# Kernel optimization log

Measured on AMD Instinct MI355X. Metric: run time of the kernel, lower is better.

## Reference

```python
import jax, jax.numpy as jnp
import numpy as np

N = 50000
E = 600000
LLM_DIM = 640
HIDDEN = 128
STRUCT_DIM = 16
N_STRUCT_TYPES = 5
N_LAYERS = 2
LN_EPS = 1e-5


def setup_inputs() -> dict:
    key = jax.random.key(0)
    ks = jax.random.split(key, 10)
    llm_feat = jax.random.normal(ks[0], (N, LLM_DIM), dtype=jnp.float32)
    struct_type_ids = jax.random.randint(ks[1], (N,), 0, N_STRUCT_TYPES, dtype=jnp.int64)
    edge_index = jax.random.randint(ks[2], (2, E), 0, N, dtype=jnp.int64)
    proj_out = HIDDEN - STRUCT_DIM  # 112
    proj_W = jax.random.normal(ks[3], (LLM_DIM, proj_out), dtype=jnp.float32) / np.sqrt(LLM_DIM)
    proj_b = jnp.zeros((proj_out,), dtype=jnp.float32)
    struct_emb = jax.random.normal(ks[4], (N_STRUCT_TYPES, STRUCT_DIM), dtype=jnp.float32)
    gcn_W = jax.random.normal(ks[5], (N_LAYERS, HIDDEN, HIDDEN), dtype=jnp.float32) / np.sqrt(HIDDEN)
    gcn_b = jnp.zeros((N_LAYERS, HIDDEN), dtype=jnp.float32)
    ln_g = jnp.ones((HIDDEN,), dtype=jnp.float32)
    ln_b = jnp.zeros((HIDDEN,), dtype=jnp.float32)
    return dict(llm_feat=llm_feat, struct_type_ids=struct_type_ids, edge_index=edge_index,
                proj_W=proj_W, proj_b=proj_b, struct_emb=struct_emb,
                gcn_W=gcn_W, gcn_b=gcn_b, ln_g=ln_g, ln_b=ln_b)


def _gcn_conv(x, src, dst, deg_inv_sqrt, W, b):
    """PyG GCNConv: x' = D^{-1/2}(A+I)D^{-1/2} (x W) + b, D over A+I."""
    xw = x @ W  # [N, H]
    norm = deg_inv_sqrt[src] * deg_inv_sqrt[dst]  # [E]
    msg = xw[src] * norm[:, None]  # [E, H]
    agg = jax.ops.segment_sum(msg, dst, num_segments=N)  # [N, H]
    # self-loop contribution: norm_ii = deg_i^{-1}
    agg = agg + xw * (deg_inv_sqrt * deg_inv_sqrt)[:, None]
    return agg + b


def reference(llm_feat, struct_type_ids, edge_index, proj_W, proj_b,
              struct_emb, gcn_W, gcn_b, ln_g, ln_b):
    x_llm = llm_feat @ proj_W + proj_b  # [N, hidden-struct_dim]
    x_struct = struct_emb[struct_type_ids]  # [N, struct_dim]
    x = jnp.concatenate([x_llm, x_struct], axis=-1)  # [N, hidden]

    src, dst = edge_index[0], edge_index[1]
    # degree with self-loops (A + I)
    deg = 1.0 + jax.ops.segment_sum(jnp.ones((E,), dtype=x.dtype), dst, num_segments=N)
    deg_inv_sqrt = jax.lax.rsqrt(deg)

    for l in range(N_LAYERS):
        x_new = jax.nn.relu(_gcn_conv(x, src, dst, deg_inv_sqrt, gcn_W[l], gcn_b[l]))
        # dropout is identity in eval mode
        x = x + x_new

    mean = jnp.mean(x, axis=-1, keepdims=True)
    var = jnp.mean(jnp.square(x - mean), axis=-1, keepdims=True)
    return (x - mean) * jax.lax.rsqrt(var + LN_EPS) * ln_g + ln_b
```

## Files before the change

kernel.cpp:

```cpp
#include <hip/hip_runtime.h>

#define N_NODES 50000
#define E_EDGES 600000
#define LLM_DIM 640
#define HIDDEN 128
#define POUT 112
#define NB_SCAN 98

typedef __attribute__((ext_vector_type(8))) short bf16x8;
typedef __attribute__((ext_vector_type(4))) float f32x4;

__device__ inline unsigned short f2bf(float f) {
    unsigned u = __float_as_uint(f);
    u += 0x7fff + ((u >> 16) & 1);
    return (unsigned short)(u >> 16);
}
__device__ inline float bflo(unsigned v) { return __uint_as_float(v << 16); }
__device__ inline float bfhi(unsigned v) { return __uint_as_float(v & 0xffff0000u); }

__global__ void deg_count(const int* __restrict__ eidx, int* __restrict__ cnt) {
    int e = blockIdx.x * 256 + threadIdx.x;
    if (e < E_EDGES) atomicAdd(&cnt[eidx[E_EDGES + e]], 1);
}

__global__ void make_dis(const int* __restrict__ cnt, float* __restrict__ dis) {
    int i = blockIdx.x * 256 + threadIdx.x;
    if (i < N_NODES) dis[i] = rsqrtf(1.0f + (float)cnt[i]);
}

__global__ __launch_bounds__(256) void scan_blocksum(const int* __restrict__ cnt, int* __restrict__ bsum) {
    __shared__ int s[256];
    int b = blockIdx.x, t = threadIdx.x;
    int i0 = b * 512 + t, i1 = i0 + 256;
    int v = (i0 < N_NODES ? cnt[i0] : 0) + (i1 < N_NODES ? cnt[i1] : 0);
    s[t] = v;
    __syncthreads();
    for (int st = 128; st; st >>= 1) {
        if (t < st) s[t] += s[t + st];
        __syncthreads();
    }
    if (t == 0) bsum[b] = s[0];
}

__global__ void scan_bsum(const int* __restrict__ bsum, int* __restrict__ bpre) {
    __shared__ int s[128];
    int t = threadIdx.x;
    if (t < NB_SCAN) s[t] = bsum[t];
    __syncthreads();
    if (t == 0) {
        int a = 0;
        for (int i = 0; i < NB_SCAN; i++) { int v = s[i]; s[i] = a; a += v; }
    }
    __syncthreads();
    if (t < NB_SCAN) bpre[t] = s[t];
}

__global__ __launch_bounds__(256) void scan_offs(const int* __restrict__ cnt, const int* __restrict__ bpre,
                                                 int* __restrict__ offs) {
    __shared__ int sA[512], sB[512];
    int b = blockIdx.x, t = threadIdx.x;
    int i0 = b * 512 + t, i1 = i0 + 256;
    int v0 = (i0 < N_NODES ? cnt[i0] : 0);
    int v1 = (i1 < N_NODES ? cnt[i1] : 0);
    sA[t] = v0; sA[t + 256] = v1;
    int* src = sA; int* dst = sB;
    for (int st = 1; st < 512; st <<= 1) {
        __syncthreads();
        dst[t]       = src[t]       + (t       >= st ? src[t - st]       : 0);
        dst[t + 256] = src[t + 256] + (t + 256 >= st ? src[t + 256 - st] : 0);
        int* tmp = src; src = dst; dst = tmp;
    }
    __syncthreads();
    int base = bpre[b];
    if (i0 < N_NODES) offs[i0] = base + src[t] - v0;
    if (i1 < N_NODES) offs[i1] = base + src[t + 256] - v1;
    if (b == 0 && t == 0) offs[N_NODES] = E_EDGES;
}

__global__ void fill_srcs(const int* __restrict__ eidx, const int* __restrict__ offs,
                          int* __restrict__ pos, int* __restrict__ srcs) {
    int e = blockIdx.x * 256 + threadIdx.x;
    if (e >= E_EDGES) return;
    int s = eidx[e];
    int d = eidx[E_EDGES + e];
    int p = atomicAdd(&pos[d], 1);
    srcs[offs[d] + p] = s;
}

__global__ void conv_weights(const float* __restrict__ Wp, const float* __restrict__ Wg,
                             unsigned short* __restrict__ Wt, unsigned short* __restrict__ Wt2) {
    int idx = blockIdx.x * 256 + threadIdx.x;
    if (idx < POUT * LLM_DIM) {
        int n = idx / LLM_DIM;
        int k = idx - n * LLM_DIM;
        Wt[(size_t)n * LLM_DIM + k] = f2bf(Wp[(size_t)k * POUT + n]);
    } else {
        int i2 = idx - POUT * LLM_DIM;
        if (i2 < 2 * HIDDEN * HIDDEN) {
            int l = i2 >> 14;
            int rem = i2 & 16383;
            int n = rem >> 7;
            int k = rem & 127;
            Wt2[i2] = f2bf(Wg[l * 16384 + k * 128 + n]);
        }
    }
}

__global__ __launch_bounds__(256) void proj_mfma(const float* __restrict__ A,
                                                 const unsigned short* __restrict__ Wt,
                                                 const float* __restrict__ bias,
                                                 const float* __restrict__ emb,
                                                 const int* __restrict__ sid,
                                                 const float* __restrict__ dis,
                                                 float* __restrict__ X,
                                                 unsigned short* __restrict__ Xs) {
    __shared__ short As[64][72];
    __shared__ short Bs[112][72];
    const int tid = threadIdx.x;
    const int wave = tid >> 6, lane = tid & 63;
    const int row0 = blockIdx.x * 64;
    const int l15 = lane & 15, l4 = lane >> 4;

    f32x4 acc[7];
#pragma unroll
    for (int j = 0; j < 7; j++) acc[j] = (f32x4){0.f, 0.f, 0.f, 0.f};

    for (int k0 = 0; k0 < LLM_DIM; k0 += 64) {
#pragma unroll
        for (int i = 0; i < 4; i++) {
            int f = i * 256 + tid;
            int r = f >> 4;
            int q = f & 15;
            int grow = row0 + r;
            float4 v = make_float4(0.f, 0.f, 0.f, 0.f);
            if (grow < N_NODES)
                v = *reinterpret_cast<const float4*>(A + (size_t)grow * LLM_DIM + k0 + q * 4);
            uint2 u;
            u.x = (unsigned)f2bf(v.x) | ((unsigned)f2bf(v.y) << 16);
            u.y = (unsigned)f2bf(v.z) | ((unsigned)f2bf(v.w) << 16);
            *reinterpret_cast<uint2*>(&As[r][q * 4]) = u;
        }
#pragma unroll
        for (int i = 0; i < 7; i++) {
            int f = i * 256 + tid;
            int n = f >> 4;
            int q = f & 15;
            uint2 v = *reinterpret_cast<const uint2*>(Wt + (size_t)n * LLM_DIM + k0 + q * 4);
            *reinterpret_cast<uint2*>(&Bs[n][q * 4]) = v;
        }
        __syncthreads();
#pragma unroll
        for (int ks = 0; ks < 2; ks++) {
            int kk = ks * 32 + l4 * 8;
            bf16x8 a = *reinterpret_cast<bf16x8*>(&As[wave * 16 + l15][kk]);
#pragma unroll
            for (int ct = 0; ct < 7; ct++) {
                bf16x8 b = *reinterpret_cast<bf16x8*>(&Bs[ct * 16 + l15][kk]);
                acc[ct] = __builtin_amdgcn_mfma_f32_16x16x32_bf16(a, b, acc[ct], 0, 0, 0);
            }
        }
        __syncthreads();
    }
#pragma unroll
    for (int r = 0; r < 4; r++) {
        int row = row0 + wave * 16 + l4 * 4 + r;
        if (row >= N_NODES) continue;
        float d = dis[row];
#pragma unroll
        for (int ct = 0; ct < 7; ct++) {
            int col = ct * 16 + l15;
            float v = acc[ct][r] + bias[col];
            X[(size_t)row * HIDDEN + col] = v;
            Xs[(size_t)row * HIDDEN + col] = f2bf(d * v);
        }
        float e = emb[sid[row] * 16 + l15];
        X[(size_t)row * HIDDEN + POUT + l15] = e;
        Xs[(size_t)row * HIDDEN + POUT + l15] = f2bf(d * e);
    }
}

__global__ __launch_bounds__(256) void gather(const unsigned short* __restrict__ Xs,
                                              const int* __restrict__ offs,
                                              const int* __restrict__ srcs,
                                              const float* __restrict__ dis,
                                              unsigned short* __restrict__ Gb) {
    int node = blockIdx.x * 4 + (threadIdx.x >> 6);
    int lane = threadIdx.x & 63;
    if (node >= N_NODES) return;
    int beg = __builtin_amdgcn_readfirstlane(offs[node]);
    int end = __builtin_amdgcn_readfirstlane(offs[node + 1]);
    const unsigned* X32 = reinterpret_cast<const unsigned*>(Xs);
    float d = dis[node];
    unsigned sv = X32[(size_t)node * 64 + lane];
    float ax = 0.f, ay = 0.f;
    int e = beg;
    while (e < end) {
        int n = end - e;
        if (n > 64) n = 64;
        int idx = (lane < n) ? srcs[e + lane] : 0;
        int j = 0;
        for (; j + 8 <= n; j += 8) {
            int s0 = __shfl(idx, j);
            int s1 = __shfl(idx, j + 1);
            int s2 = __shfl(idx, j + 2);
            int s3 = __shfl(idx, j + 3);
            int s4 = __shfl(idx, j + 4);
            int s5 = __shfl(idx, j + 5);
            int s6 = __shfl(idx, j + 6);
            int s7 = __shfl(idx, j + 7);
            unsigned v0 = X32[(size_t)s0 * 64 + lane];
            unsigned v1 = X32[(size_t)s1 * 64 + lane];
            unsigned v2 = X32[(size_t)s2 * 64 + lane];
            unsigned v3 = X32[(size_t)s3 * 64 + lane];
            unsigned v4 = X32[(size_t)s4 * 64 + lane];
            unsigned v5 = X32[(size_t)s5 * 64 + lane];
            unsigned v6 = X32[(size_t)s6 * 64 + lane];
            unsigned v7 = X32[(size_t)s7 * 64 + lane];
            ax += ((bflo(v0) + bflo(v1)) + (bflo(v2) + bflo(v3)))
                + ((bflo(v4) + bflo(v5)) + (bflo(v6) + bflo(v7)));
            ay += ((bfhi(v0) + bfhi(v1)) + (bfhi(v2) + bfhi(v3)))
                + ((bfhi(v4) + bfhi(v5)) + (bfhi(v6) + bfhi(v7)));
        }
        if (j + 4 <= n) {
            int s0 = __shfl(idx, j);
            int s1 = __shfl(idx, j + 1);
            int s2 = __shfl(idx, j + 2);
            int s3 = __shfl(idx, j + 3);
            unsigned v0 = X32[(size_t)s0 * 64 + lane];
            unsigned v1 = X32[(size_t)s1 * 64 + lane];
            unsigned v2 = X32[(size_t)s2 * 64 + lane];
            unsigned v3 = X32[(size_t)s3 * 64 + lane];
            ax += (bflo(v0) + bflo(v1)) + (bflo(v2) + bflo(v3));
            ay += (bfhi(v0) + bfhi(v1)) + (bfhi(v2) + bfhi(v3));
            j += 4;
        }
        int rem = n - j;
        if (rem > 0) {
            int s0 = __shfl(idx, j);
            int s1 = __shfl(idx, j + (rem > 1 ? 1 : 0));
            int s2 = __shfl(idx, j + (rem > 2 ? 2 : 0));
            unsigned v0 = X32[(size_t)s0 * 64 + lane];
            unsigned v1 = X32[(size_t)s1 * 64 + lane];
            unsigned v2 = X32[(size_t)s2 * 64 + lane];
            ax += bflo(v0) + (rem > 1 ? bflo(v1) : 0.f) + (rem > 2 ? bflo(v2) : 0.f);
            ay += bfhi(v0) + (rem > 1 ? bfhi(v1) : 0.f) + (rem > 2 ? bfhi(v2) : 0.f);
        }
        e += 64;
    }
    ax = d * (ax + bflo(sv));
    ay = d * (ay + bfhi(sv));
    reinterpret_cast<unsigned*>(Gb)[(size_t)node * 64 + lane] =
        (unsigned)f2bf(ax) | ((unsigned)f2bf(ay) << 16);
}

template <int MODE>
__global__ __launch_bounds__(256) void gemm_fin(const unsigned short* __restrict__ Gb,
                                                const unsigned short* __restrict__ Wt2,
                                                const float* __restrict__ bias,
                                                const float* __restrict__ dis,
                                                const float* __restrict__ lng,
                                                const float* __restrict__ lnb,
                                                float* __restrict__ X,
                                                unsigned short* __restrict__ Xs2) {
    __shared__ short As[64][136];
    __shared__ short Bs[128][136];
    const int tid = threadIdx.x;
    const int wave = tid >> 6, lane = tid & 63;
    const int row0 = blockIdx.x * 64;
    const int l15 = lane & 15, l4 = lane >> 4;

#pragma unroll
    for (int i = 0; i < 4; i++) {
        int f = i * 256 + tid;
        int r = f >> 4;
        int q = f & 15;
        int grow = row0 + r;
        uint4 v = make_uint4(0, 0, 0, 0);
        if (grow < N_NODES)
            v = reinterpret_cast<const uint4*>(Gb + (size_t)grow * HIDDEN)[q];
        *reinterpret_cast<uint4*>(&As[r][q * 8]) = v;
    }
#pragma unroll
    for (int i = 0; i < 8; i++) {
        int f = i * 256 + tid;
        int r = f >> 4;
        int q = f & 15;
        uint4 v = reinterpret_cast<const uint4*>(Wt2 + (size_t)r * HIDDEN)[q];
        *reinterpret_cast<uint4*>(&Bs[r][q * 8]) = v;
    }

    float xo[8][4];
#pragma unroll
    for (int r = 0; r < 4; r++) {
        int row = row0 + wave * 16 + l4 * 4 + r;
        int rc = row < N_NODES ? row : 0;
#pragma unroll
        for (int ct = 0; ct < 8; ct++)
            xo[ct][r] = X[(size_t)rc * HIDDEN + ct * 16 + l15];
    }

    __syncthreads();

    f32x4 acc[8];
#pragma unroll
    for (int j = 0; j < 8; j++) acc[j] = (f32x4){0.f, 0.f, 0.f, 0.f};
#pragma unroll
    for (int ks = 0; ks < 4; ks++) {
        int kk = ks * 32 + l4 * 8;
        bf16x8 a = *reinterpret_cast<bf16x8*>(&As[wave * 16 + l15][kk]);
#pragma unroll
        for (int ct = 0; ct < 8; ct++) {
            bf16x8 b = *reinterpret_cast<bf16x8*>(&Bs[ct * 16 + l15][kk]);
            acc[ct] = __builtin_amdgcn_mfma_f32_16x16x32_bf16(a, b, acc[ct], 0, 0, 0);
        }
    }

    float bcol[8];
#pragma unroll
    for (int ct = 0; ct < 8; ct++) bcol[ct] = bias[ct * 16 + l15];

    float vv[8][4];
#pragma unroll
    for (int r = 0; r < 4; r++) {
        int row = row0 + wave * 16 + l4 * 4 + r;
        bool ok = row < N_NODES;
#pragma unroll
        for (int ct = 0; ct < 8; ct++) {
            float xv = ok ? xo[ct][r] : 0.f;
            vv[ct][r] = xv + fmaxf(acc[ct][r] + bcol[ct], 0.f);
        }
    }

    if (MODE == 0) {
#pragma unroll
        for (int r = 0; r < 4; r++) {
            int row = row0 + wave * 16 + l4 * 4 + r;
            if (row >= N_NODES) continue;
            float d = dis[row];
#pragma unroll
            for (int ct = 0; ct < 8; ct++) {
                int col = ct * 16 + l15;
                X[(size_t)row * HIDDEN + col] = vv[ct][r];
                Xs2[(size_t)row * HIDDEN + col] = f2bf(d * vv[ct][r]);
            }
        }
    } else {
        float s[4], q2[4];
#pragma unroll
        for (int r = 0; r < 4; r++) {
            s[r] = 0.f; q2[r] = 0.f;
#pragma unroll
            for (int ct = 0; ct < 8; ct++) {
                s[r] += vv[ct][r];
                q2[r] += vv[ct][r] * vv[ct][r];
            }
        }
#pragma unroll
        for (int off = 1; off < 16; off <<= 1) {
#pragma unroll
            for (int r = 0; r < 4; r++) {
                s[r] += __shfl_xor(s[r], off);
                q2[r] += __shfl_xor(q2[r], off);
            }
        }
        float gcol[8], bcol2[8];
#pragma unroll
        for (int ct = 0; ct < 8; ct++) {
            gcol[ct] = lng[ct * 16 + l15];
            bcol2[ct] = lnb[ct * 16 + l15];
        }
#pragma unroll
        for (int r = 0; r < 4; r++) {
            int row = row0 + wave * 16 + l4 * 4 + r;
            if (row >= N_NODES) continue;
            float mean = s[r] * (1.f / 128.f);
            float var = q2[r] * (1.f / 128.f) - mean * mean;
            float inv = rsqrtf(var + 1e-5f);
#pragma unroll
            for (int ct = 0; ct < 8; ct++) {
                int col = ct * 16 + l15;
                X[(size_t)row * HIDDEN + col] = (vv[ct][r] - mean) * inv * gcol[ct] + bcol2[ct];
            }
        }
    }
}

extern "C" void kernel_launch(void* const* d_in, const int* in_sizes, int n_in,
                              void* d_out, int out_size, void* d_ws, size_t ws_size,
                              hipStream_t stream) {
    const float* llm   = (const float*)d_in[0];
    const int*   sid   = (const int*)d_in[1];
    const int*   eidx  = (const int*)d_in[2];
    const float* projW = (const float*)d_in[3];
    const float* projb = (const float*)d_in[4];
    const float* emb   = (const float*)d_in[5];
    const float* gcnW  = (const float*)d_in[6];
    const float* gcnb  = (const float*)d_in[7];
    const float* lng   = (const float*)d_in[8];
    const float* lnb   = (const float*)d_in[9];

    float* X = (float*)d_out;
    unsigned short* Xs = (unsigned short*)d_ws;
    unsigned short* Gb = Xs + (size_t)N_NODES * HIDDEN;
    unsigned short* Wt = Gb;
    unsigned short* Wt2 = Gb + (size_t)N_NODES * HIDDEN;
    float* dis = (float*)(Wt2 + 2 * HIDDEN * HIDDEN);
    int* cnt  = (int*)(dis + N_NODES);
    int* pos  = cnt + N_NODES;
    int* offs = pos + N_NODES;
    int* bsum = offs + N_NODES + 1;
    int* bpre = bsum + 128;
    int* srcs = bpre + 128;

    hipMemsetAsync(cnt, 0, 2 * N_NODES * sizeof(int), stream);
    deg_count<<<(E_EDGES + 255) / 256, 256, 0, stream>>>(eidx, cnt);
    make_dis<<<(N_NODES + 255) / 256, 256, 0, stream>>>(cnt, dis);
    scan_blocksum<<<NB_SCAN, 256, 0, stream>>>(cnt, bsum);
    scan_bsum<<<1, 128, 0, stream>>>(bsum, bpre);
    scan_offs<<<NB_SCAN, 256, 0, stream>>>(cnt, bpre, offs);
    fill_srcs<<<(E_EDGES + 255) / 256, 256, 0, stream>>>(eidx, offs, pos, srcs);

    conv_weights<<<(POUT * LLM_DIM + 2 * HIDDEN * HIDDEN + 255) / 256, 256, 0, stream>>>(projW, gcnW, Wt, Wt2);

    proj_mfma<<<(N_NODES + 63) / 64, 256, 0, stream>>>(llm, Wt, projb, emb, sid, dis, X, Xs);

    gather<<<(N_NODES + 3) / 4, 256, 0, stream>>>(Xs, offs, srcs, dis, Gb);
    gemm_fin<0><<<(N_NODES + 63) / 64, 256, 0, stream>>>(Gb, Wt2, gcnb, dis, lng, lnb, X, Xs);
    gather<<<(N_NODES + 3) / 4, 256, 0, stream>>>(Xs, offs, srcs, dis, Gb);
    gemm_fin<1><<<(N_NODES + 63) / 64, 256, 0, stream>>>(Gb, Wt2 + HIDDEN * HIDDEN, gcnb + HIDDEN, dis, lng, lnb, X, Xs);
}
```

Baseline: 375.1 us.

## Fuse neighbor gather into per-layer GEMM kernel with 16-lane vectorized aggregation

Removes the standalone gather kernel and its bf16 Gb intermediate. Each GCN layer kernel now aggregates its own 64 rows straight into shared memory before the MFMA GEMM. The aggregation now handles four nodes per wave, with 16 lanes per node doing 16-byte loads, instead of one node per wave with 4-byte loads. This cuts global write and read traffic and two launches. The cost is that the gather runs inside a block holding about 52KB of LDS, which limits occupancy and latency hiding for the irregular loads.

```diff
diff --git a/kernel.cpp b/kernel.cpp
--- a/kernel.cpp
+++ b/kernel.cpp
@@ -14,6 +14,9 @@
     unsigned u = __float_as_uint(f);
     u += 0x7fff + ((u >> 16) & 1);
     return (unsigned short)(u >> 16);
+}
+__device__ inline unsigned pk2(float lo, float hi) {
+    return (unsigned)f2bf(lo) | ((unsigned)f2bf(hi) << 16);
 }
 __device__ inline float bflo(unsigned v) { return __uint_as_float(v << 16); }
 __device__ inline float bfhi(unsigned v) { return __uint_as_float(v & 0xffff0000u); }
@@ -136,8 +139,8 @@
             if (grow < N_NODES)
                 v = *reinterpret_cast<const float4*>(A + (size_t)grow * LLM_DIM + k0 + q * 4);
             uint2 u;
-            u.x = (unsigned)f2bf(v.x) | ((unsigned)f2bf(v.y) << 16);
-            u.y = (unsigned)f2bf(v.z) | ((unsigned)f2bf(v.w) << 16);
+            u.x = pk2(v.x, v.y);
+            u.y = pk2(v.z, v.w);
             *reinterpret_cast<uint2*>(&As[r][q * 4]) = u;
         }
 #pragma unroll
@@ -179,89 +182,17 @@
     }
 }
 
-__global__ __launch_bounds__(256) void gather(const unsigned short* __restrict__ Xs,
-                                              const int* __restrict__ offs,
-                                              const int* __restrict__ srcs,
-                                              const float* __restrict__ dis,
-                                              unsigned short* __restrict__ Gb) {
-    int node = blockIdx.x * 4 + (threadIdx.x >> 6);
-    int lane = threadIdx.x & 63;
-    if (node >= N_NODES) return;
-    int beg = __builtin_amdgcn_readfirstlane(offs[node]);
-    int end = __builtin_amdgcn_readfirstlane(offs[node + 1]);
-    const unsigned* X32 = reinterpret_cast<const unsigned*>(Xs);
-    float d = dis[node];
-    unsigned sv = X32[(size_t)node * 64 + lane];
-    float ax = 0.f, ay = 0.f;
-    int e = beg;
-    while (e < end) {
-        int n = end - e;
-        if (n > 64) n = 64;
-        int idx = (lane < n) ? srcs[e + lane] : 0;
-        int j = 0;
-        for (; j + 8 <= n; j += 8) {
-            int s0 = __shfl(idx, j);
-            int s1 = __shfl(idx, j + 1);
-            int s2 = __shfl(idx, j + 2);
-            int s3 = __shfl(idx, j + 3);
-            int s4 = __shfl(idx, j + 4);
-            int s5 = __shfl(idx, j + 5);
-            int s6 = __shfl(idx, j + 6);
-            int s7 = __shfl(idx, j + 7);
-            unsigned v0 = X32[(size_t)s0 * 64 + lane];
-            unsigned v1 = X32[(size_t)s1 * 64 + lane];
-            unsigned v2 = X32[(size_t)s2 * 64 + lane];
-            unsigned v3 = X32[(size_t)s3 * 64 + lane];
-            unsigned v4 = X32[(size_t)s4 * 64 + lane];
-            unsigned v5 = X32[(size_t)s5 * 64 + lane];
-            unsigned v6 = X32[(size_t)s6 * 64 + lane];
-            unsigned v7 = X32[(size_t)s7 * 64 + lane];
-            ax += ((bflo(v0) + bflo(v1)) + (bflo(v2) + bflo(v3)))
-                + ((bflo(v4) + bflo(v5)) + (bflo(v6) + bflo(v7)));
-            ay += ((bfhi(v0) + bfhi(v1)) + (bfhi(v2) + bfhi(v3)))
-                + ((bfhi(v4) + bfhi(v5)) + (bfhi(v6) + bfhi(v7)));
-        }
-        if (j + 4 <= n) {
-            int s0 = __shfl(idx, j);
-            int s1 = __shfl(idx, j + 1);
-            int s2 = __shfl(idx, j + 2);
-            int s3 = __shfl(idx, j + 3);
-            unsigned v0 = X32[(size_t)s0 * 64 + lane];
-            unsigned v1 = X32[(size_t)s1 * 64 + lane];
-            unsigned v2 = X32[(size_t)s2 * 64 + lane];
-            unsigned v3 = X32[(size_t)s3 * 64 + lane];
-            ax += (bflo(v0) + bflo(v1)) + (bflo(v2) + bflo(v3));
-            ay += (bfhi(v0) + bfhi(v1)) + (bfhi(v2) + bfhi(v3));
-            j += 4;
-        }
-        int rem = n - j;
-        if (rem > 0) {
-            int s0 = __shfl(idx, j);
-            int s1 = __shfl(idx, j + (rem > 1 ? 1 : 0));
-            int s2 = __shfl(idx, j + (rem > 2 ? 2 : 0));
-            unsigned v0 = X32[(size_t)s0 * 64 + lane];
-            unsigned v1 = X32[(size_t)s1 * 64 + lane];
-            unsigned v2 = X32[(size_t)s2 * 64 + lane];
-            ax += bflo(v0) + (rem > 1 ? bflo(v1) : 0.f) + (rem > 2 ? bflo(v2) : 0.f);
-            ay += bfhi(v0) + (rem > 1 ? bfhi(v1) : 0.f) + (rem > 2 ? bfhi(v2) : 0.f);
-        }
-        e += 64;
-    }
-    ax = d * (ax + bflo(sv));
-    ay = d * (ay + bfhi(sv));
-    reinterpret_cast<unsigned*>(Gb)[(size_t)node * 64 + lane] =
-        (unsigned)f2bf(ax) | ((unsigned)f2bf(ay) << 16);
-}
-
 template <int MODE>
-__global__ __launch_bounds__(256) void gemm_fin(const unsigned short* __restrict__ Gb,
-                                                const unsigned short* __restrict__ Wt2,
-                                                const float* __restrict__ bias,
-                                                const float* __restrict__ dis,
-                                                const float* __restrict__ lng,
-                                                const float* __restrict__ lnb,
-                                                float* __restrict__ X,
-                                                unsigned short* __restrict__ Xs2) {
+__global__ __launch_bounds__(256) void gcn_layer(const unsigned short* __restrict__ XsIn,
+                                                 const int* __restrict__ offs,
+                                                 const int* __restrict__ srcs,
+                                                 const float* __restrict__ dis,
+                                                 const unsigned short* __restrict__ Wt2,
+                                                 const float* __restrict__ bias,
+                                                 const float* __restrict__ lng,
+                                                 const float* __restrict__ lnb,
+                                                 float* __restrict__ X,
+                                                 unsigned short* __restrict__ XsOut) {
     __shared__ short As[64][136];
     __shared__ short Bs[128][136];
     const int tid = threadIdx.x;
@@ -270,17 +201,6 @@
     const int l15 = lane & 15, l4 = lane >> 4;
 
 #pragma unroll
-    for (int i = 0; i < 4; i++) {
-        int f = i * 256 + tid;
-        int r = f >> 4;
-        int q = f & 15;
-        int grow = row0 + r;
-        uint4 v = make_uint4(0, 0, 0, 0);
-        if (grow < N_NODES)
-            v = reinterpret_cast<const uint4*>(Gb + (size_t)grow * HIDDEN)[q];
-        *reinterpret_cast<uint4*>(&As[r][q * 8]) = v;
-    }
-#pragma unroll
     for (int i = 0; i < 8; i++) {
         int f = i * 256 + tid;
         int r = f >> 4;
@@ -289,6 +209,102 @@
         *reinterpret_cast<uint4*>(&Bs[r][q * 8]) = v;
     }
 
+    const int sub = lane >> 4;
+    const int sl  = lane & 15;
+    const uint4* X4 = reinterpret_cast<const uint4*>(XsIn);
+    unsigned* AsU = reinterpret_cast<unsigned*>(&As[0][0]);
+
+#pragma unroll 1
+    for (int g = 0; g < 4; g++) {
+        int trow = wave * 16 + g * 4 + sub;
+        int node = row0 + trow;
+        float a0 = 0.f, a1 = 0.f, a2 = 0.f, a3 = 0.f;
+        float b0 = 0.f, b1 = 0.f, b2 = 0.f, b3 = 0.f;
+        if (node < N_NODES) {
+            int beg = offs[node];
+            int end = offs[node + 1];
+            float dn = dis[node];
+            uint4 sv = X4[(size_t)node * 16 + sl];
+            for (int e0 = beg; e0 < end; e0 += 16) {
+                int m = end - e0; if (m > 16) m = 16;
+                int idx = (sl < m) ? srcs[e0 + sl] : 0;
+                int j = 0;
+                for (; j + 8 <= m; j += 8) {
+                    int s0 = __shfl(idx, j, 16),     s1 = __shfl(idx, j + 1, 16);
+                    int s2 = __shfl(idx, j + 2, 16), s3 = __shfl(idx, j + 3, 16);
+                    int s4 = __shfl(idx, j + 4, 16), s5 = __shfl(idx, j + 5, 16);
+                    int s6 = __shfl(idx, j + 6, 16), s7 = __shfl(idx, j + 7, 16);
+                    uint4 v0 = X4[(size_t)s0 * 16 + sl];
+                    uint4 v1 = X4[(size_t)s1 * 16 + sl];
+                    uint4 v2 = X4[(size_t)s2 * 16 + sl];
+                    uint4 v3 = X4[(size_t)s3 * 16 + sl];
+                    uint4 v4 = X4[(size_t)s4 * 16 + sl];
+                    uint4 v5 = X4[(size_t)s5 * 16 + sl];
+                    uint4 v6 = X4[(size_t)s6 * 16 + sl];
+                    uint4 v7 = X4[(size_t)s7 * 16 + sl];
+                    a0 += ((bflo(v0.x) + bflo(v1.x)) + (bflo(v2.x) + bflo(v3.x)))
+                        + ((bflo(v4.x) + bflo(v5.x)) + (bflo(v6.x) + bflo(v7.x)));
+                    b0 += ((bfhi(v0.x) + bfhi(v1.x)) + (bfhi(v2.x) + bfhi(v3.x)))
+                        + ((bfhi(v4.x) + bfhi(v5.x)) + (bfhi(v6.x) + bfhi(v7.x)));
+                    a1 += ((bflo(v0.y) + bflo(v1.y)) + (bflo(v2.y) + bflo(v3.y)))
+                        + ((bflo(v4.y) + bflo(v5.y)) + (bflo(v6.y) + bflo(v7.y)));
+                    b1 += ((bfhi(v0.y) + bfhi(v1.y)) + (bfhi(v2.y) + bfhi(v3.y)))
+                        + ((bfhi(v4.y) + bfhi(v5.y)) + (bfhi(v6.y) + bfhi(v7.y)));
+                    a2 += ((bflo(v0.z) + bflo(v1.z)) + (bflo(v2.z) + bflo(v3.z)))
+                        + ((bflo(v4.z) + bflo(v5.z)) + (bflo(v6.z) + bflo(v7.z)));
+                    b2 += ((bfhi(v0.z) + bfhi(v1.z)) + (bfhi(v2.z) + bfhi(v3.z)))
+                        + ((bfhi(v4.z) + bfhi(v5.z)) + (bfhi(v6.z) + bfhi(v7.z)));
+                    a3 += ((bflo(v0.w) + bflo(v1.w)) + (bflo(v2.w) + bflo(v3.w)))
+                        + ((bflo(v4.w) + bflo(v5.w)) + (bflo(v6.w) + bflo(v7.w)));
+                    b3 += ((bfhi(v0.w) + bfhi(v1.w)) + (bfhi(v2.w) + bfhi(v3.w)))
+                        + ((bfhi(v4.w) + bfhi(v5.w)) + (bfhi(v6.w) + bfhi(v7.w)));
+                }
+                if (j + 4 <= m) {
+                    int s0 = __shfl(idx, j, 16),     s1 = __shfl(idx, j + 1, 16);
+                    int s2 = __shfl(idx, j + 2, 16), s3 = __shfl(idx, j + 3, 16);
+                    uint4 v0 = X4[(size_t)s0 * 16 + sl];
+                    uint4 v1 = X4[(size_t)s1 * 16 + sl];
+                    uint4 v2 = X4[(size_t)s2 * 16 + sl];
+                    uint4 v3 = X4[(size_t)s3 * 16 + sl];
+                    a0 += (bflo(v0.x) + bflo(v1.x)) + (bflo(v2.x) + bflo(v3.x));
+                    b0 += (bfhi(v0.x) + bfhi(v1.x)) + (bfhi(v2.x) + bfhi(v3.x));
+                    a1 += (bflo(v0.y) + bflo(v1.y)) + (bflo(v2.y) + bflo(v3.y));
+                    b1 += (bfhi(v0.y) + bfhi(v1.y)) + (bfhi(v2.y) + bfhi(v3.y));
+                    a2 += (bflo(v0.z) + bflo(v1.z)) + (bflo(v2.z) + bflo(v3.z));
+                    b2 += (bfhi(v0.z) + bfhi(v1.z)) + (bfhi(v2.z) + bfhi(v3.z));
+                    a3 += (bflo(v0.w) + bflo(v1.w)) + (bflo(v2.w) + bflo(v3.w));
+                    b3 += (bfhi(v0.w) + bfhi(v1.w)) + (bfhi(v2.w) + bfhi(v3.w));
+                    j += 4;
+                }
+                int rem = m - j;
+                if (rem > 0) {
+                    int s0 = __shfl(idx, j, 16);
+                    int s1 = __shfl(idx, j + (rem > 1 ? 1 : 0), 16);
+                    int s2 = __shfl(idx, j + (rem > 2 ? 2 : 0), 16);
+                    uint4 v0 = X4[(size_t)s0 * 16 + sl];
+                    uint4 v1 = X4[(size_t)s1 * 16 + sl];
+                    uint4 v2 = X4[(size_t)s2 * 16 + sl];
+                    float m1 = rem > 1 ? 1.f : 0.f, m2 = rem > 2 ? 1.f : 0.f;
+                    a0 += bflo(v0.x) + m1 * bflo(v1.x) + m2 * bflo(v2.x);
+                    b0 += bfhi(v0.x) + m1 * bfhi(v1.x) + m2 * bfhi(v2.x);
+                    a1 += bflo(v0.y) + m1 * bflo(v1.y) + m2 * bflo(v2.y);
+                    b1 += bfhi(v0.y) + m1 * bfhi(v1.y) + m2 * bfhi(v2.y);
+                    a2 += bflo(v0.z) + m1 * bflo(v1.z) + m2 * bflo(v2.z);
+                    b2 += bfhi(v0.z) + m1 * bfhi(v1.z) + m2 * bfhi(v2.z);
+                    a3 += bflo(v0.w) + m1 * bflo(v1.w) + m2 * bflo(v2.w);
+                    b3 += bfhi(v0.w) + m1 * bfhi(v1.w) + m2 * bfhi(v2.w);
+                }
+            }
+            a0 = dn * (a0 + bflo(sv.x)); b0 = dn * (b0 + bfhi(sv.x));
+            a1 = dn * (a1 + bflo(sv.y)); b1 = dn * (b1 + bfhi(sv.y));
+            a2 = dn * (a2 + bflo(sv.z)); b2 = dn * (b2 + bfhi(sv.z));
+            a3 = dn * (a3 + bflo(sv.w)); b3 = dn * (b3 + bfhi(sv.w));
+        }
+        uint4 w;
+        w.x = pk2(a0, b0); w.y = pk2(a1, b1); w.z = pk2(a2, b2); w.w = pk2(a3, b3);
+        *reinterpret_cast<uint4*>(&AsU[trow * 68 + sl * 4]) = w;
+    }
+
     float xo[8][4];
 #pragma unroll
     for (int r = 0; r < 4; r++) {
@@ -341,7 +357,7 @@
             for (int ct = 0; ct < 8; ct++) {
                 int col = ct * 16 + l15;
                 X[(size_t)row * HIDDEN + col] = vv[ct][r];
-                Xs2[(size_t)row * HIDDEN + col] = f2bf(d * vv[ct][r]);
+                XsOut[(size_t)row * HIDDEN + col] = f2bf(d * vv[ct][r]);
             }
         }
     } else {
@@ -400,10 +416,10 @@
     const float* lnb   = (const float*)d_in[9];
 
     float* X = (float*)d_out;
-    unsigned short* Xs = (unsigned short*)d_ws;
-    unsigned short* Gb = Xs + (size_t)N_NODES * HIDDEN;
-    unsigned short* Wt = Gb;
-    unsigned short* Wt2 = Gb + (size_t)N_NODES * HIDDEN;
+    unsigned short* Xsa = (unsigned short*)d_ws;
+    unsigned short* Xsb = Xsa + (size_t)N_NODES * HIDDEN;
+    unsigned short* Wt = Xsb;
+    unsigned short* Wt2 = Xsb + (size_t)N_NODES * HIDDEN;
     float* dis = (float*)(Wt2 + 2 * HIDDEN * HIDDEN);
     int* cnt  = (int*)(dis + N_NODES);
     int* pos  = cnt + N_NODES;
@@ -422,10 +438,10 @@
 
     conv_weights<<<(POUT * LLM_DIM + 2 * HIDDEN * HIDDEN + 255) / 256, 256, 0, stream>>>(projW, gcnW, Wt, Wt2);
 
-    proj_mfma<<<(N_NODES + 63) / 64, 256, 0, stream>>>(llm, Wt, projb, emb, sid, dis, X, Xs);
-
-    gather<<<(N_NODES + 3) / 4, 256, 0, stream>>>(Xs, offs, srcs, dis, Gb);
-    gemm_fin<0><<<(N_NODES + 63) / 64, 256, 0, stream>>>(Gb, Wt2, gcnb, dis, lng, lnb, X, Xs);
-    gather<<<(N_NODES + 3) / 4, 256, 0, stream>>>(Xs, offs, srcs, dis, Gb);
-    gemm_fin<1><<<(N_NODES + 63) / 64, 256, 0, stream>>>(Gb, Wt2 + HIDDEN * HIDDEN, gcnb + HIDDEN, dis, lng, lnb, X, Xs);
-}
+    proj_mfma<<<(N_NODES + 63) / 64, 256, 0, stream>>>(llm, Wt, projb, emb, sid, dis, X, Xsa);
+
+    gcn_layer<0><<<(N_NODES + 63) / 64, 256, 0, stream>>>(Xsa, offs, srcs, dis, Wt2, gcnb,
+                                                          lng, lnb, X, Xsb);
+    gcn_layer<1><<<(N_NODES + 63) / 64, 256, 0, stream>>>(Xsb, offs, srcs, dis, Wt2 + HIDDEN * HIDDEN,
+                                                          gcnb + HIDDEN, lng, lnb, X, Xsb);
+}
```

Result: slower. 384.2 us (+2.4%).

## Carry degree-scaled bf16 features as residual state and fuse small setup kernels

Applied to the files above, without the earlier changes.

Drops the fp32 feature matrix X between layers. Only the bf16 copy pre-scaled by deg^-1/2 is kept, and the residual is rebuilt from it with the scale applied to the relu term. LayerNorm's epsilon is rescaled by d^2 so the final normalization stays equivalent. It also folds make_dis into scan_blocksum and merges fill_srcs with the weight conversion into one launch, cutting launches and fp32 global traffic. In exchange the residual path now runs at bf16 precision, which may add numerical error.

```diff
diff --git a/kernel.cpp b/kernel.cpp
--- a/kernel.cpp
+++ b/kernel.cpp
@@ -6,6 +6,9 @@
 #define HIDDEN 128
 #define POUT 112
 #define NB_SCAN 98
+#define FILL_BLOCKS 2344
+#define CONV_ELEMS (POUT * LLM_DIM + 2 * HIDDEN * HIDDEN)
+#define CONV_BLOCKS 408
 
 typedef __attribute__((ext_vector_type(8))) short bf16x8;
 typedef __attribute__((ext_vector_type(4))) float f32x4;
@@ -23,17 +26,16 @@
     if (e < E_EDGES) atomicAdd(&cnt[eidx[E_EDGES + e]], 1);
 }
 
-__global__ void make_dis(const int* __restrict__ cnt, float* __restrict__ dis) {
-    int i = blockIdx.x * 256 + threadIdx.x;
-    if (i < N_NODES) dis[i] = rsqrtf(1.0f + (float)cnt[i]);
-}
-
-__global__ __launch_bounds__(256) void scan_blocksum(const int* __restrict__ cnt, int* __restrict__ bsum) {
+__global__ __launch_bounds__(256) void scan_blocksum(const int* __restrict__ cnt, int* __restrict__ bsum,
+                                                     float* __restrict__ dis) {
     __shared__ int s[256];
     int b = blockIdx.x, t = threadIdx.x;
     int i0 = b * 512 + t, i1 = i0 + 256;
-    int v = (i0 < N_NODES ? cnt[i0] : 0) + (i1 < N_NODES ? cnt[i1] : 0);
-    s[t] = v;
+    int c0 = (i0 < N_NODES ? cnt[i0] : 0);
+    int c1 = (i1 < N_NODES ? cnt[i1] : 0);
+    if (i0 < N_NODES) dis[i0] = rsqrtf(1.0f + (float)c0);
+    if (i1 < N_NODES) dis[i1] = rsqrtf(1.0f + (float)c1);
+    s[t] = c0 + c1;
     __syncthreads();
     for (int st = 128; st; st >>= 1) {
         if (t < st) s[t] += s[t + st];
@@ -77,26 +79,26 @@
     if (b == 0 && t == 0) offs[N_NODES] = E_EDGES;
 }
 
-__global__ void fill_srcs(const int* __restrict__ eidx, const int* __restrict__ offs,
-                          int* __restrict__ pos, int* __restrict__ srcs) {
-    int e = blockIdx.x * 256 + threadIdx.x;
-    if (e >= E_EDGES) return;
-    int s = eidx[e];
-    int d = eidx[E_EDGES + e];
-    int p = atomicAdd(&pos[d], 1);
-    srcs[offs[d] + p] = s;
-}
-
-__global__ void conv_weights(const float* __restrict__ Wp, const float* __restrict__ Wg,
-                             unsigned short* __restrict__ Wt, unsigned short* __restrict__ Wt2) {
-    int idx = blockIdx.x * 256 + threadIdx.x;
-    if (idx < POUT * LLM_DIM) {
-        int n = idx / LLM_DIM;
-        int k = idx - n * LLM_DIM;
-        Wt[(size_t)n * LLM_DIM + k] = f2bf(Wp[(size_t)k * POUT + n]);
+__global__ void fill_and_conv(const int* __restrict__ eidx, const int* __restrict__ offs,
+                              int* __restrict__ pos, int* __restrict__ srcs,
+                              const float* __restrict__ Wp, const float* __restrict__ Wg,
+                              unsigned short* __restrict__ Wt, unsigned short* __restrict__ Wt2) {
+    int b = blockIdx.x;
+    if (b < FILL_BLOCKS) {
+        int e = b * 256 + threadIdx.x;
+        if (e >= E_EDGES) return;
+        int s = eidx[e];
+        int d = eidx[E_EDGES + e];
+        int p = atomicAdd(&pos[d], 1);
+        srcs[offs[d] + p] = s;
     } else {
-        int i2 = idx - POUT * LLM_DIM;
-        if (i2 < 2 * HIDDEN * HIDDEN) {
+        int idx = (b - FILL_BLOCKS) * 256 + threadIdx.x;
+        if (idx < POUT * LLM_DIM) {
+            int n = idx / LLM_DIM;
+            int k = idx - n * LLM_DIM;
+            Wt[(size_t)n * LLM_DIM + k] = f2bf(Wp[(size_t)k * POUT + n]);
+        } else if (idx < CONV_ELEMS) {
+            int i2 = idx - POUT * LLM_DIM;
             int l = i2 >> 14;
             int rem = i2 & 16383;
             int n = rem >> 7;
@@ -112,7 +114,6 @@
                                                  const float* __restrict__ emb,
                                                  const int* __restrict__ sid,
                                                  const float* __restrict__ dis,
-                                                 float* __restrict__ X,
                                                  unsigned short* __restrict__ Xs) {
     __shared__ short As[64][72];
     __shared__ short Bs[112][72];
@@ -169,12 +170,9 @@
 #pragma unroll
         for (int ct = 0; ct < 7; ct++) {
             int col = ct * 16 + l15;
-            float v = acc[ct][r] + bias[col];
-            X[(size_t)row * HIDDEN + col] = v;
-            Xs[(size_t)row * HIDDEN + col] = f2bf(d * v);
+            Xs[(size_t)row * HIDDEN + col] = f2bf(d * (acc[ct][r] + bias[col]));
         }
         float e = emb[sid[row] * 16 + l15];
-        X[(size_t)row * HIDDEN + POUT + l15] = e;
         Xs[(size_t)row * HIDDEN + POUT + l15] = f2bf(d * e);
     }
 }
@@ -260,8 +258,9 @@
                                                 const float* __restrict__ dis,
                                                 const float* __restrict__ lng,
                                                 const float* __restrict__ lnb,
+                                                const unsigned short* XsIn,
                                                 float* __restrict__ X,
-                                                unsigned short* __restrict__ Xs2) {
+                                                unsigned short* XsOut) {
     __shared__ short As[64][136];
     __shared__ short Bs[128][136];
     const int tid = threadIdx.x;
@@ -289,14 +288,20 @@
         *reinterpret_cast<uint4*>(&Bs[r][q * 8]) = v;
     }
 
-    float xo[8][4];
+    const unsigned* XsU = reinterpret_cast<const unsigned*>(XsIn);
+    float xs[8][4];
+    float dv[4];
 #pragma unroll
     for (int r = 0; r < 4; r++) {
         int row = row0 + wave * 16 + l4 * 4 + r;
         int rc = row < N_NODES ? row : 0;
-#pragma unroll
-        for (int ct = 0; ct < 8; ct++)
-            xo[ct][r] = X[(size_t)rc * HIDDEN + ct * 16 + l15];
+        dv[r] = dis[rc];
+        bool hi = (l15 & 1) != 0;
+#pragma unroll
+        for (int ct = 0; ct < 8; ct++) {
+            unsigned u = XsU[(size_t)rc * 64 + ct * 8 + (l15 >> 1)];
+            xs[ct][r] = hi ? bfhi(u) : bflo(u);
+        }
     }
 
     __syncthreads();
@@ -322,13 +327,9 @@
     float vv[8][4];
 #pragma unroll
     for (int r = 0; r < 4; r++) {
-        int row = row0 + wave * 16 + l4 * 4 + r;
-        bool ok = row < N_NODES;
-#pragma unroll
-        for (int ct = 0; ct < 8; ct++) {
-            float xv = ok ? xo[ct][r] : 0.f;
-            vv[ct][r] = xv + fmaxf(acc[ct][r] + bcol[ct], 0.f);
-        }
+#pragma unroll
+        for (int ct = 0; ct < 8; ct++)
+            vv[ct][r] = xs[ct][r] + dv[r] * fmaxf(acc[ct][r] + bcol[ct], 0.f);
     }
 
     if (MODE == 0) {
@@ -336,13 +337,9 @@
         for (int r = 0; r < 4; r++) {
             int row = row0 + wave * 16 + l4 * 4 + r;
             if (row >= N_NODES) continue;
-            float d = dis[row];
-#pragma unroll
-            for (int ct = 0; ct < 8; ct++) {
-                int col = ct * 16 + l15;
-                X[(size_t)row * HIDDEN + col] = vv[ct][r];
-                Xs2[(size_t)row * HIDDEN + col] = f2bf(d * vv[ct][r]);
-            }
+#pragma unroll
+            for (int ct = 0; ct < 8; ct++)
+                XsOut[(size_t)row * HIDDEN + ct * 16 + l15] = f2bf(vv[ct][r]);
         }
     } else {
         float s[4], q2[4];
@@ -375,7 +372,7 @@
             if (row >= N_NODES) continue;
             float mean = s[r] * (1.f / 128.f);
             float var = q2[r] * (1.f / 128.f) - mean * mean;
-            float inv = rsqrtf(var + 1e-5f);
+            float inv = rsqrtf(var + 1e-5f * dv[r] * dv[r]);
 #pragma unroll
             for (int ct = 0; ct < 8; ct++) {
                 int col = ct * 16 + l15;
@@ -413,19 +410,18 @@
     int* srcs = bpre + 128;
 
     hipMemsetAsync(cnt, 0, 2 * N_NODES * sizeof(int), stream);
-    deg_count<<<(E_EDGES + 255) / 256, 256, 0, stream>>>(eidx, cnt);
-    make_dis<<<(N_NODES + 255) / 256, 256, 0, stream>>>(cnt, dis);
-    scan_blocksum<<<NB_SCAN, 256, 0, stream>>>(cnt, bsum);
+    deg_count<<<FILL_BLOCKS, 256, 0, stream>>>(eidx, cnt);
+    scan_blocksum<<<NB_SCAN, 256, 0, stream>>>(cnt, bsum, dis);
     scan_bsum<<<1, 128, 0, stream>>>(bsum, bpre);
     scan_offs<<<NB_SCAN, 256, 0, stream>>>(cnt, bpre, offs);
-    fill_srcs<<<(E_EDGES + 255) / 256, 256, 0, stream>>>(eidx, offs, pos, srcs);
-
-    conv_weights<<<(POUT * LLM_DIM + 2 * HIDDEN * HIDDEN + 255) / 256, 256, 0, stream>>>(projW, gcnW, Wt, Wt2);
-
-    proj_mfma<<<(N_NODES + 63) / 64, 256, 0, stream>>>(llm, Wt, projb, emb, sid, dis, X, Xs);
+    fill_and_conv<<<FILL_BLOCKS + CONV_BLOCKS, 256, 0, stream>>>(eidx, offs, pos, srcs,
+                                                                 projW, gcnW, Wt, Wt2);
+
+    proj_mfma<<<(N_NODES + 63) / 64, 256, 0, stream>>>(llm, Wt, projb, emb, sid, dis, Xs);
 
     gather<<<(N_NODES + 3) / 4, 256, 0, stream>>>(Xs, offs, srcs, dis, Gb);
-    gemm_fin<0><<<(N_NODES + 63) / 64, 256, 0, stream>>>(Gb, Wt2, gcnb, dis, lng, lnb, X, Xs);
+    gemm_fin<0><<<(N_NODES + 63) / 64, 256, 0, stream>>>(Gb, Wt2, gcnb, dis, lng, lnb, Xs, X, Xs);
     gather<<<(N_NODES + 3) / 4, 256, 0, stream>>>(Xs, offs, srcs, dis, Gb);
-    gemm_fin<1><<<(N_NODES + 63) / 64, 256, 0, stream>>>(Gb, Wt2 + HIDDEN * HIDDEN, gcnb + HIDDEN, dis, lng, lnb, X, Xs);
-}
+    gemm_fin<1><<<(N_NODES + 63) / 64, 256, 0, stream>>>(Gb, Wt2 + HIDDEN * HIDDEN, gcnb + HIDDEN,
+                                                         dis, lng, lnb, Xs, X, Xs);
+}
```

After: 364.5 us. 2.8% less time.
